# Performance work log

Measured on AMD Instinct MI355X. Metric: run time of the kernel, lower is better.

## Reference

```python
import jax, jax.numpy as jnp
import numpy as np

B, T, IN, H, OUT = 128, 512, 64, 1024, 1


def _glorot(key, shape, fan_in):
    # mimic nn.Linear default init scale (uniform +-1/sqrt(fan_in))
    bound = 1.0 / np.sqrt(fan_in)
    return jax.random.uniform(key, shape, jnp.float32, -bound, bound)


def setup_inputs() -> dict:
    key = jax.random.key(0)
    ks = jax.random.split(key, 20)
    inp = {
        "x": jax.random.normal(ks[0], (B, T, IN), jnp.float32),
        "boundary": jax.random.normal(ks[1], (B, 2), jnp.float32),
        # layer 0: stacked gate weights, order [i, f, o, g]
        "Wx0": _glorot(ks[2], (4 * H, IN), IN),
        "bx0": _glorot(ks[3], (4 * H,), IN),
        "Uh0": _glorot(ks[4], (4 * H, H), H),
        "bh0": _glorot(ks[5], (4 * H,), H),
        "Wb0": _glorot(ks[6], (H, 2), 2),
        "bb0": _glorot(ks[7], (H,), 2),
        # layer 1
        "Wx1": _glorot(ks[8], (4 * H, H), H),
        "bx1": _glorot(ks[9], (4 * H,), H),
        "Uh1": _glorot(ks[10], (4 * H, H), H),
        "bh1": _glorot(ks[11], (4 * H,), H),
        "Wb1": _glorot(ks[12], (H, 2), 2),
        "bb1": _glorot(ks[13], (H, 2)[:1], 2),
        # output head
        "fcW": _glorot(ks[14], (OUT, H), H),
        "fcb": _glorot(ks[15], (OUT,), H),
    }
    return inp


def _cell(gates, f_extra, c_prev):
    # gates: [B, 4H] pre-activations in order i,f,o,g
    i, f, o, g = jnp.split(gates, 4, axis=-1)
    i = jax.nn.sigmoid(i)
    f = jax.nn.sigmoid(f + f_extra)
    o = jax.nn.sigmoid(o)
    g = jnp.tanh(g)
    c = f * c_prev + i * g
    h = o * jnp.tanh(c)
    return h, c


def reference(x, boundary, Wx0, bx0, Uh0, bh0, Wb0, bb0,
              Wx1, bx1, Uh1, bh1, Wb1, bb1, fcW, fcb):
    batch = x.shape[0]
    Hdim = fcW.shape[1]
    # precompute input projections for layer 0 over all timesteps: [T,B,4H]
    xp0 = jnp.einsum('bti,gi->tbg', x, Wx0) + bx0
    # boundary influence on forget gate, constant over time: [B,H]
    bi0 = boundary @ Wb0.T + bb0
    bi1 = boundary @ Wb1.T + bb1

    zeros = jnp.zeros((batch, Hdim), x.dtype)
    carry0 = (zeros, zeros, zeros, zeros)  # h0, c0, h1, c1

    def step(carry, xp_t):
        h0, c0, h1, c1 = carry
        g0 = xp_t + h0 @ Uh0.T + bh0
        h0n, c0n = _cell(g0, bi0, c0)
        g1 = h0n @ Wx1.T + bx1 + h1 @ Uh1.T + bh1
        h1n, c1n = _cell(g1, bi1, c1)
        return (h0n, c0n, h1n, c1n), None

    (h0, c0, h1, c1), _ = jax.lax.scan(step, carry0, xp0)
    # fc applied to last timestep's top-layer hidden state
    return h1 @ fcW.T + fcb
```

## Files before the change

### kernel.cpp

```cpp
#include <hip/hip_runtime.h>
#include <math.h>


#define Hd 1024
#define Bd 128
#define Td 512
#define INd 64
#define NWG 256
#define NTHR 1024

typedef _Float16 f16;
typedef _Float16 half8 __attribute__((ext_vector_type(8)));
typedef float f32x4 __attribute__((ext_vector_type(4)));


__device__ __forceinline__ float fsigm(float x) {
    return __fdividef(1.f, 1.f + __expf(-x));
}
__device__ __forceinline__ float ftanh_(float x) {
    return 1.f - __fdividef(2.f, 1.f + __expf(2.f * x));
}

__global__ __launch_bounds__(512) void init_state(
    const float* __restrict__ bnd, const float* __restrict__ Wb0,
    const float* __restrict__ bb0, const float* __restrict__ Wb1,
    const float* __restrict__ bb1,
    float* __restrict__ bi0, float* __restrict__ bi1,
    f16* __restrict__ h0buf, f16* __restrict__ h1buf,
    unsigned int* __restrict__ sync)
{
    int idx = blockIdx.x * 512 + threadIdx.x;
    int b = idx >> 10;
    int h = idx & 1023;
    float b0v = bnd[b * 2 + 0], b1v = bnd[b * 2 + 1];
    bi0[idx] = b0v * Wb0[h * 2 + 0] + b1v * Wb0[h * 2 + 1] + bb0[h];
    bi1[idx] = b0v * Wb1[h * 2 + 0] + b1v * Wb1[h * 2 + 1] + bb1[h];
    h0buf[idx] = (f16)0.f;  h0buf[idx + Bd * Hd] = (f16)0.f;
    h1buf[idx] = (f16)0.f;  h1buf[idx + Bd * Hd] = (f16)0.f;
    if (idx < 640) sync[idx] = 0u;
}

__global__ __launch_bounds__(512) void xpose(
    const float* __restrict__ x, f16* __restrict__ xT)
{
    int idx = blockIdx.x * 512 + threadIdx.x;
    int b = idx >> 15;
    int t = (idx >> 6) & 511;
    int i = idx & 63;
    xT[((size_t)t * Bd + b) * INd + i] = (f16)x[idx];
}

__global__ __launch_bounds__(NTHR, 4) void lstm_persist(
    const f16* __restrict__ xT,
    f16* __restrict__ h0buf, f16* __restrict__ h1buf,
    const float* __restrict__ bi0, const float* __restrict__ bi1,
    const float* __restrict__ Wx0, const float* __restrict__ bx0,
    const float* __restrict__ Uh0, const float* __restrict__ bh0,
    const float* __restrict__ Wx1, const float* __restrict__ bx1,
    const float* __restrict__ Uh1, const float* __restrict__ bh1,
    const float* __restrict__ fcW, const float* __restrict__ fcb,
    float* __restrict__ out, unsigned int* __restrict__ sync)
{
    const int tid  = threadIdx.x;
    const int w    = tid >> 6;
    const int lane = tid & 63;
    const int n    = lane & 15;
    const int q    = lane >> 4;
    const int wg   = blockIdx.x;
    const int c0wg = wg * 4;
    const int hcol = c0wg + (n & 3);
    const int gid  = n >> 2;
    const bool lowhalf = (w < 8);
    const int p    = lowhalf ? w : (w - 8);
    const size_t S = (size_t)Bd * Hd;

    __shared__ f16 WL0[34 * 512];
    __shared__ f16 WX1[32 * 512];
    __shared__ f16 WU1[32 * 512];
    __shared__ float xchg[2048];

    const bool glead = ((wg & 31) == 0);
    unsigned int* garr = sync + 32 + 32 * (wg >> 5);
    int  xcd  = 0;
    bool lead = false;
    unsigned int* relp = nullptr;
    if (tid == 0) {
        asm volatile("s_getreg_b32 %0, hwreg(HW_REG_XCC_ID)" : "=s"(xcd));
        xcd &= 7;
        unsigned r = __hip_atomic_fetch_add(&sync[608 + xcd], 1u,
                         __ATOMIC_RELAXED, __HIP_MEMORY_SCOPE_AGENT);
        lead = (r == 0u);
        relp = sync + 288 + 32 * xcd;
    }

    for (int c = tid; c < 34 * 64; c += NTHR) {
        int kk = c >> 6, l = c & 63, qq = l >> 4, nn = l & 15;
        int gr = (nn >> 2) * Hd + c0wg + (nn & 3);
        int k0 = qq * 8 + kk * 32;
        f16* dst = &WL0[c * 8];
        if (k0 < Hd) {
            #pragma unroll
            for (int j = 0; j < 8; ++j)
                dst[j] = (f16)Uh0[(size_t)gr * Hd + k0 + j];
        } else {
            #pragma unroll
            for (int j = 0; j < 8; ++j)
                dst[j] = (f16)Wx0[(size_t)gr * INd + (k0 - Hd) + j];
        }
    }
    for (int c = tid; c < 32 * 64; c += NTHR) {
        int kk = c >> 6, l = c & 63, qq = l >> 4, nn = l & 15;
        int gr = (nn >> 2) * Hd + c0wg + (nn & 3);
        int k0 = qq * 8 + kk * 32;
        f16* d1 = &WX1[c * 8];
        f16* d2 = &WU1[c * 8];
        #pragma unroll
        for (int j = 0; j < 8; ++j) {
            d1[j] = (f16)Wx1[(size_t)gr * Hd + k0 + j];
            d2[j] = (f16)Uh1[(size_t)gr * Hd + k0 + j];
        }
    }

    float gbx[4], bia[4];
    {
        const float* bxp = lowhalf ? bx0 : bx1;
        const float* bhp = lowhalf ? bh0 : bh1;
        const float* bip = lowhalf ? bi0 : bi1;
        #pragma unroll
        for (int g = 0; g < 4; ++g)
            gbx[g] = bxp[g * Hd + hcol] + bhp[g * Hd + hcol];
        #pragma unroll
        for (int r = 0; r < 4; ++r)
            bia[r] = bip[(size_t)(p * 16 + q * 4 + r) * Hd + hcol];
    }
    f32x4 cst = {0.f, 0.f, 0.f, 0.f};

    __syncthreads();

    unsigned epoch = 0;

    for (int s = -1; s <= 511; ++s) {
        const bool do_l0 = (s < 511);
        const bool do_l1 = (s >= 0);
        const int pr = s & 1;
        const f16* h0r = h0buf + (size_t)pr * S;
        f16*       h0w = h0buf + (size_t)(1 - pr) * S;
        const f16* h1r = h1buf + (size_t)(1 - pr) * S;
        f16*       h1w = h1buf + (size_t)pr * S;

        f32x4 a0 = {0.f,0.f,0.f,0.f};
        f32x4 a1 = {0.f,0.f,0.f,0.f};

        if (lowhalf) {
            const half8* pA  = (const half8*)(h0r + (size_t)(p*16 + n) * Hd + q*8);
            const half8* pB0 = (const half8*)WL0 + lane;
            const half8* pB1 = (const half8*)WX1 + lane;
            if (do_l0 && do_l1) {
                #pragma unroll 8
                for (int kk = 0; kk < 32; ++kk) {
                    half8 A = pA[kk*4];
                    a0 = __builtin_amdgcn_mfma_f32_16x16x32_f16(A, pB0[kk*64], a0, 0,0,0);
                    a1 = __builtin_amdgcn_mfma_f32_16x16x32_f16(A, pB1[kk*64], a1, 0,0,0);
                }
            } else if (do_l0) {
                #pragma unroll 8
                for (int kk = 0; kk < 32; ++kk) {
                    half8 A = pA[kk*4];
                    a0 = __builtin_amdgcn_mfma_f32_16x16x32_f16(A, pB0[kk*64], a0, 0,0,0);
                }
            } else {
                #pragma unroll 8
                for (int kk = 0; kk < 32; ++kk) {
                    half8 A = pA[kk*4];
                    a1 = __builtin_amdgcn_mfma_f32_16x16x32_f16(A, pB1[kk*64], a1, 0,0,0);
                }
            }
            if (do_l0) {
                const f16* xt = xT + (size_t)(s + 1) * Bd * INd;
                const half8* pX = (const half8*)(xt + (size_t)(p*16 + n) * INd + q*8);
                #pragma unroll
                for (int kk = 0; kk < 2; ++kk)
                    a0 = __builtin_amdgcn_mfma_f32_16x16x32_f16(
                             pX[kk*4], pB0[(32 + kk) * 64], a0, 0,0,0);
            }
        } else if (do_l1) {
            const half8* pA  = (const half8*)(h1r + (size_t)(p*16 + n) * Hd + q*8);
            const half8* pB1 = (const half8*)WU1 + lane;
            #pragma unroll 8
            for (int kk = 0; kk < 32; ++kk) {
                half8 A = pA[kk*4];
                a1 = __builtin_amdgcn_mfma_f32_16x16x32_f16(A, pB1[kk*64], a1, 0,0,0);
            }
        }

        if (lowhalf && do_l1)
            *(f32x4*)&xchg[p * 256 + lane * 4] = a1;
        __syncthreads();
        f32x4 g1;
        if (!lowhalf && do_l1)
            g1 = a1 + *(const f32x4*)&xchg[p * 256 + lane * 4];

        auto cell = [&](f32x4 acc, f16* hw) {
            #pragma unroll
            for (int r = 0; r < 4; ++r) {
                float own = acc[r];
                float v4  = __shfl_xor(own, 4);
                float v8  = __shfl_xor(own, 8);
                float v12 = __shfl_xor(own, 12);
                float ip = gid==0?own: gid==1?v4 : gid==2?v8 : v12;
                float fp = gid==0?v4 : gid==1?own: gid==2?v12: v8;
                float op = gid==0?v8 : gid==1?v12: gid==2?own: v4;
                float gp = gid==0?v12: gid==1?v8 : gid==2?v4 : own;
                float I = fsigm(ip + gbx[0]);
                float F = fsigm(fp + gbx[1] + bia[r]);
                float O = fsigm(op + gbx[2]);
                float G = ftanh_(gp + gbx[3]);
                float c = F * cst[r] + I * G;
                cst[r] = c;
                float h = O * ftanh_(c);
                if (n < 4) {
                    union { f16 hf; unsigned short us; } cv; cv.hf = (f16)h;
                    __hip_atomic_store(
                        (unsigned short*)&hw[(size_t)(p * 16 + q * 4 + r) * Hd + c0wg + n],
                        cv.us, __ATOMIC_RELAXED, __HIP_MEMORY_SCOPE_AGENT);
                }
            }
        };
        if (lowhalf) { if (do_l0) cell(a0, h0w); }
        else         { if (do_l1) cell(g1, h1w); }

        __syncthreads();
        if (tid == 0) {
            const unsigned tgt = epoch + 1u;
            __hip_atomic_fetch_add(garr, 1u, __ATOMIC_RELAXED,
                                   __HIP_MEMORY_SCOPE_AGENT);
            if (glead) {
                while (__hip_atomic_load(garr, __ATOMIC_RELAXED,
                                         __HIP_MEMORY_SCOPE_AGENT) < 32u * tgt)
                    __builtin_amdgcn_s_sleep(1);
                __hip_atomic_fetch_add(sync, 32u, __ATOMIC_RELAXED,
                                       __HIP_MEMORY_SCOPE_AGENT);
            }
            if (lead) {
                while (__hip_atomic_load(sync, __ATOMIC_RELAXED,
                                         __HIP_MEMORY_SCOPE_AGENT) < NWG * tgt)
                    __builtin_amdgcn_s_sleep(1);
                asm volatile("buffer_inv sc1\n\ts_waitcnt vmcnt(0)" ::: "memory");
                __hip_atomic_store(relp, tgt, __ATOMIC_RELAXED,
                                   __HIP_MEMORY_SCOPE_AGENT);
            } else {
                while (__hip_atomic_load(relp, __ATOMIC_RELAXED,
                                         __HIP_MEMORY_SCOPE_AGENT) < tgt)
                    __builtin_amdgcn_s_sleep(1);
                asm volatile("buffer_inv\n\ts_waitcnt vmcnt(0)" ::: "memory");
            }
        }
        epoch++;
        __syncthreads();
    }

    if (blockIdx.x < Bd) {
        int b = blockIdx.x;
        if (tid < 512) {
            const f16* hf = h1buf + S + (size_t)b * Hd;
            int k = tid * 2;
            float sum = (float)hf[k] * fcW[k] + (float)hf[k + 1] * fcW[k + 1];
            #pragma unroll
            for (int off = 32; off > 0; off >>= 1) sum += __shfl_down(sum, off);
            if (lane == 0) xchg[w] = sum;
        }
        __syncthreads();
        if (tid == 0) {
            float t = 0.f;
            #pragma unroll
            for (int i = 0; i < 8; ++i) t += xchg[i];
            out[b] = t + fcb[0];
        }
    }
}

extern "C" void kernel_launch(void* const* d_in, const int* in_sizes, int n_in,
                              void* d_out, int out_size, void* d_ws, size_t ws_size,
                              hipStream_t stream) {
    const float* x        = (const float*)d_in[0];
    const float* boundary = (const float*)d_in[1];
    const float* Wx0      = (const float*)d_in[2];
    const float* bx0      = (const float*)d_in[3];
    const float* Uh0      = (const float*)d_in[4];
    const float* bh0      = (const float*)d_in[5];
    const float* Wb0      = (const float*)d_in[6];
    const float* bb0      = (const float*)d_in[7];
    const float* Wx1      = (const float*)d_in[8];
    const float* bx1      = (const float*)d_in[9];
    const float* Uh1      = (const float*)d_in[10];
    const float* bh1      = (const float*)d_in[11];
    const float* Wb1      = (const float*)d_in[12];
    const float* bb1      = (const float*)d_in[13];
    const float* fcW      = (const float*)d_in[14];
    const float* fcb      = (const float*)d_in[15];
    float* out = (float*)d_out;

    char* ws = (char*)d_ws;
    f16*   xT    = (f16*)(ws);
    f16*   h0buf = (f16*)(ws + 8388608);
    f16*   h1buf = (f16*)(ws + 8912896);
    float* bi0   = (float*)(ws + 9437184);
    float* bi1   = (float*)(ws + 9961472);
    unsigned int* sync = (unsigned int*)(ws + 10485760);

    init_state<<<256, 512, 0, stream>>>(boundary, Wb0, bb0, Wb1, bb1,
                                        bi0, bi1, h0buf, h1buf, sync);
    xpose<<<8192, 512, 0, stream>>>(x, xT);

    void* args[] = {
        (void*)&xT, (void*)&h0buf, (void*)&h1buf, (void*)&bi0, (void*)&bi1,
        (void*)&Wx0, (void*)&bx0, (void*)&Uh0, (void*)&bh0,
        (void*)&Wx1, (void*)&bx1, (void*)&Uh1, (void*)&bh1,
        (void*)&fcW, (void*)&fcb, (void*)&out, (void*)&sync
    };
    hipLaunchCooperativeKernel((void*)lstm_persist, dim3(NWG), dim3(NTHR),
                               args, 0, stream);
}
```

Baseline: 10.47 ms.

## Replace hierarchical atomic-counter grid barrier with per-WG flag array polled by wavefront

The grid-wide barrier used to run through two levels of fetch-add counters: group leaders summed 32 workgroups each, then per-XCD leaders waited on a global counter. Now each workgroup stores its epoch into its own flag slot, and one wavefront in each per-XCD leader workgroup polls all 256 flags in parallel (4 per lane) before releasing its XCD. This removes the serialized atomic RMW contention and the extra hierarchy hop from every timestep. In exchange, eight wavefronts now repeatedly poll 256 flag words.

```diff
diff --git a/kernel.cpp b/kernel.cpp
--- a/kernel.cpp
+++ b/kernel.cpp
@@ -37,7 +37,7 @@
     bi1[idx] = b0v * Wb1[h * 2 + 0] + b1v * Wb1[h * 2 + 1] + bb1[h];
     h0buf[idx] = (f16)0.f;  h0buf[idx + Bd * Hd] = (f16)0.f;
     h1buf[idx] = (f16)0.f;  h1buf[idx + Bd * Hd] = (f16)0.f;
-    if (idx < 640) sync[idx] = 0u;
+    if (idx < 1536) sync[idx] = 0u;
 }
 
 __global__ __launch_bounds__(512) void xpose(
@@ -78,20 +78,19 @@
     __shared__ f16 WX1[32 * 512];
     __shared__ f16 WU1[32 * 512];
     __shared__ float xchg[2048];
-
-    const bool glead = ((wg & 31) == 0);
-    unsigned int* garr = sync + 32 + 32 * (wg >> 5);
+    __shared__ int metaLead;
+
     int  xcd  = 0;
-    bool lead = false;
     unsigned int* relp = nullptr;
     if (tid == 0) {
         asm volatile("s_getreg_b32 %0, hwreg(HW_REG_XCC_ID)" : "=s"(xcd));
         xcd &= 7;
         unsigned r = __hip_atomic_fetch_add(&sync[608 + xcd], 1u,
                          __ATOMIC_RELAXED, __HIP_MEMORY_SCOPE_AGENT);
-        lead = (r == 0u);
+        metaLead = (r == 0u) ? 1 : 0;
         relp = sync + 288 + 32 * xcd;
     }
+    unsigned int* const arrf = sync + 1024;
 
     for (int c = tid; c < 34 * 64; c += NTHR) {
         int kk = c >> 6, l = c & 63, qq = l >> 4, nn = l & 15;
@@ -136,6 +135,7 @@
     f32x4 cst = {0.f, 0.f, 0.f, 0.f};
 
     __syncthreads();
+    const bool leadWG = (metaLead != 0);
 
     unsigned epoch = 0;
 
@@ -230,25 +230,34 @@
         else         { if (do_l1) cell(g1, h1w); }
 
         __syncthreads();
-        if (tid == 0) {
+        {
             const unsigned tgt = epoch + 1u;
-            __hip_atomic_fetch_add(garr, 1u, __ATOMIC_RELAXED,
+            if (tid == 0)
+                __hip_atomic_store(&arrf[wg], tgt, __ATOMIC_RELAXED,
                                    __HIP_MEMORY_SCOPE_AGENT);
-            if (glead) {
-                while (__hip_atomic_load(garr, __ATOMIC_RELAXED,
-                                         __HIP_MEMORY_SCOPE_AGENT) < 32u * tgt)
-                    __builtin_amdgcn_s_sleep(1);
-                __hip_atomic_fetch_add(sync, 32u, __ATOMIC_RELAXED,
-                                       __HIP_MEMORY_SCOPE_AGENT);
-            }
-            if (lead) {
-                while (__hip_atomic_load(sync, __ATOMIC_RELAXED,
-                                         __HIP_MEMORY_SCOPE_AGENT) < NWG * tgt)
-                    __builtin_amdgcn_s_sleep(1);
-                asm volatile("buffer_inv sc1\n\ts_waitcnt vmcnt(0)" ::: "memory");
-                __hip_atomic_store(relp, tgt, __ATOMIC_RELAXED,
-                                   __HIP_MEMORY_SCOPE_AGENT);
-            } else {
+            if (leadWG) {
+                if (w == 0) {
+                    const unsigned int* af = arrf + lane * 4;
+                    for (;;) {
+                        unsigned f0 = __hip_atomic_load(&af[0], __ATOMIC_RELAXED,
+                                          __HIP_MEMORY_SCOPE_AGENT);
+                        unsigned f1 = __hip_atomic_load(&af[1], __ATOMIC_RELAXED,
+                                          __HIP_MEMORY_SCOPE_AGENT);
+                        unsigned f2 = __hip_atomic_load(&af[2], __ATOMIC_RELAXED,
+                                          __HIP_MEMORY_SCOPE_AGENT);
+                        unsigned f3 = __hip_atomic_load(&af[3], __ATOMIC_RELAXED,
+                                          __HIP_MEMORY_SCOPE_AGENT);
+                        unsigned mn = min(min(f0, f1), min(f2, f3));
+                        if (__all(mn >= tgt)) break;
+                        __builtin_amdgcn_s_sleep(1);
+                    }
+                    if (lane == 0) {
+                        asm volatile("buffer_inv sc1\n\ts_waitcnt vmcnt(0)" ::: "memory");
+                        __hip_atomic_store(relp, tgt, __ATOMIC_RELAXED,
+                                           __HIP_MEMORY_SCOPE_AGENT);
+                    }
+                }
+            } else if (tid == 0) {
                 while (__hip_atomic_load(relp, __ATOMIC_RELAXED,
                                          __HIP_MEMORY_SCOPE_AGENT) < tgt)
                     __builtin_amdgcn_s_sleep(1);
```

Measured after the change: 10.73 ms. 2.5% more time.
